# Optimization experiments

Measured on AMD Instinct MI355X. Metric: run time of the kernel, lower is better.

The kernel has to match this reference:

```python
import jax, jax.numpy as jnp
import numpy as np
from functools import partial

B, T, F = 4096, 256, 32
H1, H2, NT = 64, 32, 3


def _lstm_layer(x, W_ih, W_hh, b_ih, b_hh):
    """Torch-style LSTM (batch_first). x: [B,T,Fin], W_ih: [4H,Fin], W_hh: [4H,H].
    Gate order i, f, g, o. Returns all hidden states [B,T,H]."""
    Bsz = x.shape[0]
    H = W_hh.shape[1]
    # Precompute input contribution for all timesteps (one big GEMM)
    xg = jnp.einsum('btf,gf->btg', x, W_ih) + b_ih + b_hh  # [B,T,4H]

    def step(carry, xg_t):
        h, c = carry
        gates = xg_t + h @ W_hh.T  # [B,4H]
        i, f, g, o = jnp.split(gates, 4, axis=-1)
        i = jax.nn.sigmoid(i)
        f = jax.nn.sigmoid(f)
        g = jnp.tanh(g)
        o = jax.nn.sigmoid(o)
        c = f * c + i * g
        h = o * jnp.tanh(c)
        return (h, c), h

    init = (jnp.zeros((Bsz, H), x.dtype), jnp.zeros((Bsz, H), x.dtype))
    _, hs = jax.lax.scan(step, init, jnp.swapaxes(xg, 0, 1))  # hs: [T,B,H]
    return jnp.swapaxes(hs, 0, 1)


def setup_inputs() -> dict:
    key = jax.random.key(0)
    ks = jax.random.split(key, 12)
    s1 = 1.0 / np.sqrt(H1)
    s2 = 1.0 / np.sqrt(H2)
    u = lambda k, shape, s: jax.random.uniform(k, shape, jnp.float32, -s, s)
    return {
        'x': jax.random.normal(ks[0], (B, T, F), jnp.float32),
        'W_ih1': u(ks[1], (4 * H1, F), s1),
        'W_hh1': u(ks[2], (4 * H1, H1), s1),
        'b_ih1': u(ks[3], (4 * H1,), s1),
        'b_hh1': u(ks[4], (4 * H1,), s1),
        'W_ih2': u(ks[5], (4 * H2, H1), s2),
        'W_hh2': u(ks[6], (4 * H2, H2), s2),
        'b_ih2': u(ks[7], (4 * H2,), s2),
        'b_hh2': u(ks[8], (4 * H2,), s2),
        'W_head': u(ks[9], (NT, H2), s2),
        'b_head': u(ks[10], (NT,), s2),
    }


def reference(x, W_ih1, W_hh1, b_ih1, b_hh1, W_ih2, W_hh2, b_ih2, b_hh2, W_head, b_head):
    h1 = _lstm_layer(x, W_ih1, W_hh1, b_ih1, b_hh1)   # [B,T,64]; dropout is identity in eval
    h2 = _lstm_layer(h1, W_ih2, W_hh2, b_ih2, b_hh2)  # [B,T,32]
    last = h2[:, -1, :]                               # [B,32]
    return last @ W_head.T + b_head                   # [B,3]
```

## Files before the change

kernel.cpp:

```cpp
#include <hip/hip_runtime.h>

#define Bsz 4096
#define Tt  256
#define Ff  32
#define H1  64
#define H2  32
#define NTAPS 3
#define BT  8
#define NTHR 256

typedef _Float16 half8  __attribute__((ext_vector_type(8)));
typedef float    f32x4  __attribute__((ext_vector_type(4)));

#define H1S 72
#define XS  40
#define H2S 40
#define HDS 33

__device__ __forceinline__ float lstm_unit(float pi, float pf, float pg, float po,
                                           float& c) {
    const float K1 = 1.4426950408889634f;
    float ei = __builtin_amdgcn_exp2f(-K1 * pi);
    float ef = __builtin_amdgcn_exp2f(-K1 * pf);
    float eg = __builtin_amdgcn_exp2f(-2.0f * K1 * __builtin_fabsf(pg));
    float eo = __builtin_amdgcn_exp2f(-K1 * po);
    float f_ = __builtin_amdgcn_rcpf(1.0f + ef);
    float ig = (1.0f - eg) * __builtin_amdgcn_rcpf((1.0f + ei) * (1.0f + eg));
    ig = __builtin_copysignf(ig, pg);
    c = f_ * c + ig;
    float ec = __builtin_amdgcn_exp2f(-2.0f * K1 * __builtin_fabsf(c));
    float th = (1.0f - ec) * __builtin_amdgcn_rcpf((1.0f + eo) * (1.0f + ec));
    return __builtin_copysignf(th, c);
}

#define MFMA16(a, b, c) __builtin_amdgcn_mfma_f32_16x16x32_f16((a), (b), (c), 0, 0, 0)

__global__ __launch_bounds__(NTHR, 2)
void lstm2_fused(const float* __restrict__ x,
                 const float* __restrict__ Wih1, const float* __restrict__ Whh1,
                 const float* __restrict__ bih1, const float* __restrict__ bhh1,
                 const float* __restrict__ Wih2, const float* __restrict__ Whh2,
                 const float* __restrict__ bih2, const float* __restrict__ bhh2,
                 const float* __restrict__ Whead, const float* __restrict__ bhead,
                 float* __restrict__ out)
{
    __shared__ __align__(16) _Float16 sH1[2][BT][H1S];
    __shared__ __align__(16) _Float16 sX [2][BT][XS];
    __shared__ __align__(16) _Float16 sH2[2][BT][H2S];
    __shared__ __align__(16) float    sHead[BT][HDS];

    const int tid  = threadIdx.x;
    const int wid  = tid >> 6;
    const int lane = tid & 63;
    const int l15  = lane & 15;
    const int q    = lane >> 4;
    const int row8 = l15 & 7;
    const int b0   = blockIdx.x * BT;

    const int colL1 = wid * 16 + l15;
    const int r0  = (q >> 1) * 2, r1 = r0 + 1;
    const int bLo = (q & 1) * 4 + (q >> 1) * 2;
    const int hT   = wid >> 1, wpar = wid & 1;
    const int hL2  = hT * 16 + l15;
    const int rL2  = 2 * wpar + (q >> 1);
    const int bL2  = (q & 1) * 4 + 2 * wpar + (q >> 1);

    half8 w1[4][3], w2[4][3];
    float bias1[4], bias2[4];
    #pragma unroll
    for (int G = 0; G < 4; ++G) {
        int gr1 = G * 64 + wid * 16 + l15;
        int gr2 = G * 32 + hT * 16 + l15;
        #pragma unroll
        for (int c = 0; c < 3; ++c) {
            half8 v1, v2;
            #pragma unroll
            for (int e = 0; e < 8; ++e) {
                int k = c * 32 + q * 8 + e;
                float f1 = (k < H1) ? Whh1[gr1 * H1 + k] : Wih1[gr1 * Ff + (k - H1)];
                int kk = q * 8 + e;
                float f2 = (c == 0) ? Whh2[gr2 * H2 + kk]
                                    : Wih2[gr2 * H1 + (c - 1) * 32 + kk];
                v1[e] = (_Float16)f1; v2[e] = (_Float16)f2;
            }
            w1[G][c] = v1; w2[G][c] = v2;
        }
        bias1[G] = bih1[gr1] + bhh1[gr1];
        bias2[G] = bih2[gr2] + bhh2[gr2];
    }

    for (int idx = tid; idx < BT * H1S; idx += NTHR) ((_Float16*)sH1[1])[idx] = (_Float16)0.0f;
    for (int idx = tid; idx < BT * H2S; idx += NTHR) ((_Float16*)sH2[1])[idx] = (_Float16)0.0f;

    const int xb = tid >> 5, xf = tid & 31;
    float rA, rB;
    {
        const float* xp = x + ((size_t)(b0 + xb) * Tt) * Ff + xf;
        sX[0][xb][xf] = (_Float16)xp[0];
        rA = xp[1 * Ff];
        rB = xp[2 * Ff];
    }
    __syncthreads();

    float cs0 = 0.0f, cs1 = 0.0f, cs2 = 0.0f;

    for (int i = 0; i <= Tt; ++i) {
        const int cur = i & 1, nxt = cur ^ 1;

        half8 a0 = *(const half8*)&sH1[nxt][row8][q * 8];
        half8 a1 = *(const half8*)&sH1[nxt][row8][32 + q * 8];

        if (i < Tt) {
            half8 ax = *(const half8*)&sX[cur][row8][q * 8];
            f32x4 acc[4];
            #pragma unroll
            for (int G = 0; G < 4; ++G) {
                f32x4 a = {bias1[G], bias1[G], bias1[G], bias1[G]};
                a = MFMA16(a0, w1[G][0], a);
                a = MFMA16(a1, w1[G][1], a);
                a = MFMA16(ax, w1[G][2], a);
                acc[G] = a;
            }
            float h0  = lstm_unit(acc[0][r0], acc[1][r0], acc[2][r0], acc[3][r0], cs0);
            float h1v = lstm_unit(acc[0][r1], acc[1][r1], acc[2][r1], acc[3][r1], cs1);
            sH1[cur][bLo][colL1]     = (_Float16)h0;
            sH1[cur][bLo + 1][colL1] = (_Float16)h1v;
        }
        if (i >= 1) {
            half8 ah = *(const half8*)&sH2[cur][row8][q * 8];
            f32x4 acc[4];
            #pragma unroll
            for (int G = 0; G < 4; ++G) {
                f32x4 a = {bias2[G], bias2[G], bias2[G], bias2[G]};
                a = MFMA16(ah, w2[G][0], a);
                a = MFMA16(a0, w2[G][1], a);
                a = MFMA16(a1, w2[G][2], a);
                acc[G] = a;
            }
            float h2v = lstm_unit(acc[0][rL2], acc[1][rL2], acc[2][rL2], acc[3][rL2], cs2);
            sH2[nxt][bL2][hL2] = (_Float16)h2v;
            if (i == Tt) sHead[bL2][hL2] = h2v;
        }

        if (i + 1 < Tt) sX[nxt][xb][xf] = (_Float16)rA;
        rA = rB;
        {
            int tld = (i + 3 < Tt) ? (i + 3) : (Tt - 1);
            rB = x[((size_t)(b0 + xb) * Tt + tld) * Ff + xf];
        }
        __syncthreads();
    }

    if (tid < BT * NTAPS) {
        int b = tid / NTAPS, n = tid - b * NTAPS;
        float s = bhead[n];
        #pragma unroll
        for (int k = 0; k < H2; ++k) s = fmaf(sHead[b][k], Whead[n * H2 + k], s);
        out[(size_t)(b0 + b) * NTAPS + n] = s;
    }
}

extern "C" void kernel_launch(void* const* d_in, const int* in_sizes, int n_in,
                              void* d_out, int out_size, void* d_ws, size_t ws_size,
                              hipStream_t stream) {
    const float* xp    = (const float*)d_in[0];
    const float* Wih1  = (const float*)d_in[1];
    const float* Whh1  = (const float*)d_in[2];
    const float* bih1  = (const float*)d_in[3];
    const float* bhh1  = (const float*)d_in[4];
    const float* Wih2  = (const float*)d_in[5];
    const float* Whh2  = (const float*)d_in[6];
    const float* bih2  = (const float*)d_in[7];
    const float* bhh2  = (const float*)d_in[8];
    const float* Whead = (const float*)d_in[9];
    const float* bhead = (const float*)d_in[10];
    float* outp = (float*)d_out;

    hipLaunchKernelGGL(lstm2_fused, dim3(Bsz / BT), dim3(NTHR), 0, stream,
                       xp, Wih1, Whh1, bih1, bhh1, Wih2, Whh2, bih2, bhh2,
                       Whead, bhead, outp);
}
```

Measured before the change: 443.7 us.

## Stream x into LDS in 16-step chunks via async global_load_lds DMA

Replaces the per-timestep register prefetch of x (one scalar global load and one fp16 LDS store per thread per step) with double-buffered chunks of 16 timesteps. Each chunk is loaded straight into LDS as fp32 with global_load_lds 16-byte DMA, issued once every 16 steps. The fp16 conversion moves to the MFMA operand build via cvt_pkrtz. This takes global-load issue and the store-to-LDS work off the serial recurrence path. In exchange it uses more LDS (fp32 chunk buffers) and relies on the barrier and waitcnt ordering to make the DMA data visible before it is read.

```diff
diff --git a/kernel.cpp b/kernel.cpp
--- a/kernel.cpp
+++ b/kernel.cpp
@@ -8,12 +8,13 @@
 #define NTAPS 3
 #define BT  8
 #define NTHR 256
+#define CH  16
 
 typedef _Float16 half8  __attribute__((ext_vector_type(8)));
+typedef __fp16   fp16x2 __attribute__((ext_vector_type(2)));
 typedef float    f32x4  __attribute__((ext_vector_type(4)));
 
 #define H1S 72
-#define XS  40
 #define H2S 40
 #define HDS 33
 
@@ -35,6 +36,12 @@
 
 #define MFMA16(a, b, c) __builtin_amdgcn_mfma_f32_16x16x32_f16((a), (b), (c), 0, 0, 0)
 
+__device__ __forceinline__ void dma16(const float* gp, const float* lp) {
+    __builtin_amdgcn_global_load_lds(
+        (const __attribute__((address_space(1))) void*)gp,
+        (__attribute__((address_space(3))) void*)lp, 16, 0, 0);
+}
+
 __global__ __launch_bounds__(NTHR, 2)
 void lstm2_fused(const float* __restrict__ x,
                  const float* __restrict__ Wih1, const float* __restrict__ Whh1,
@@ -45,8 +52,8 @@
                  float* __restrict__ out)
 {
     __shared__ __align__(16) _Float16 sH1[2][BT][H1S];
-    __shared__ __align__(16) _Float16 sX [2][BT][XS];
     __shared__ __align__(16) _Float16 sH2[2][BT][H2S];
+    __shared__ __align__(16) float    sXC[2][CH][8][8][4];
     __shared__ __align__(16) float    sHead[BT][HDS];
 
     const int tid  = threadIdx.x;
@@ -64,6 +71,16 @@
     const int hL2  = hT * 16 + l15;
     const int rL2  = 2 * wpar + (q >> 1);
     const int bL2  = (q & 1) * 4 + 2 * wpar + (q >> 1);
+
+    const int bL  = lane & 7;
+    const int f4L = lane >> 3;
+    const float* gbase = x + (size_t)(b0 + bL) * Tt * Ff + f4L * 4;
+
+    #pragma unroll
+    for (int j = 0; j < 4; ++j) {
+        int t = (wid << 2) | j;
+        dma16(gbase + (size_t)t * Ff, &sXC[0][t][0][0][0]);
+    }
 
     half8 w1[4][3], w2[4][3];
     float bias1[4], bias2[4];
@@ -92,33 +109,33 @@
     for (int idx = tid; idx < BT * H1S; idx += NTHR) ((_Float16*)sH1[1])[idx] = (_Float16)0.0f;
     for (int idx = tid; idx < BT * H2S; idx += NTHR) ((_Float16*)sH2[1])[idx] = (_Float16)0.0f;
 
-    const int xb = tid >> 5, xf = tid & 31;
-    float rA, rB;
-    {
-        const float* xp = x + ((size_t)(b0 + xb) * Tt) * Ff + xf;
-        sX[0][xb][xf] = (_Float16)xp[0];
-        rA = xp[1 * Ff];
-        rB = xp[2 * Ff];
-    }
     __syncthreads();
 
     float cs0 = 0.0f, cs1 = 0.0f, cs2 = 0.0f;
 
     for (int i = 0; i <= Tt; ++i) {
         const int cur = i & 1, nxt = cur ^ 1;
+        const int t16 = i & (CH - 1), cbuf = (i >> 4) & 1;
 
         half8 a0 = *(const half8*)&sH1[nxt][row8][q * 8];
         half8 a1 = *(const half8*)&sH1[nxt][row8][32 + q * 8];
 
         if (i < Tt) {
-            half8 ax = *(const half8*)&sX[cur][row8][q * 8];
+            f32x4 lo = *(const f32x4*)&sXC[cbuf][t16][2 * q][row8][0];
+            f32x4 hi = *(const f32x4*)&sXC[cbuf][t16][2 * q + 1][row8][0];
+            union { half8 v; fp16x2 h[4]; } axu;
+            axu.h[0] = __builtin_amdgcn_cvt_pkrtz(lo[0], lo[1]);
+            axu.h[1] = __builtin_amdgcn_cvt_pkrtz(lo[2], lo[3]);
+            axu.h[2] = __builtin_amdgcn_cvt_pkrtz(hi[0], hi[1]);
+            axu.h[3] = __builtin_amdgcn_cvt_pkrtz(hi[2], hi[3]);
+
             f32x4 acc[4];
             #pragma unroll
             for (int G = 0; G < 4; ++G) {
                 f32x4 a = {bias1[G], bias1[G], bias1[G], bias1[G]};
                 a = MFMA16(a0, w1[G][0], a);
                 a = MFMA16(a1, w1[G][1], a);
-                a = MFMA16(ax, w1[G][2], a);
+                a = MFMA16(axu.v, w1[G][2], a);
                 acc[G] = a;
             }
             float h0  = lstm_unit(acc[0][r0], acc[1][r0], acc[2][r0], acc[3][r0], cs0);
@@ -142,11 +159,13 @@
             if (i == Tt) sHead[bL2][hL2] = h2v;
         }
 
-        if (i + 1 < Tt) sX[nxt][xb][xf] = (_Float16)rA;
-        rA = rB;
-        {
-            int tld = (i + 3 < Tt) ? (i + 3) : (Tt - 1);
-            rB = x[((size_t)(b0 + xb) * Tt + tld) * Ff + xf];
+        if ((i & (CH - 1)) == 0 && i + CH < Tt) {
+            const float* gb = gbase + (size_t)(i + CH) * Ff;
+            #pragma unroll
+            for (int j = 0; j < 4; ++j) {
+                int t = (wid << 2) | j;
+                dma16(gb + (size_t)t * Ff, &sXC[cbuf ^ 1][t][0][0][0]);
+            }
         }
         __syncthreads();
     }
```

Result: faster. 416.0 us (-6.3%).
